# Kernel optimization log

Measured on AMD Instinct MI355X. Metric: run time of the kernel, lower is better.

The kernel has to match this reference:

```python
import jax, jax.numpy as jnp
import numpy as np

D_MODEL = 512; FPQ = 15; SEQ = 2048; BSZ = 2
D_STATE = 16; D_CONV = 4; HEADDIM = 64; NHEADS = 16
D_INNER = 1024; CONV_DIM = D_INNER + 2 * D_STATE
D_IN_PROJ = 2 * D_INNER + 2 * D_STATE + NHEADS  # 2096
D_FF = 2048  # mlp_ratio 4.0 * 512
EPS_GATE = 0.01


def _rmsnorm(x, w, eps):
    xf = x.astype(jnp.float32)
    v = jnp.mean(xf * xf, axis=-1, keepdims=True)
    return w * (xf * jax.lax.rsqrt(v + eps)).astype(x.dtype)


def _mamba2(x, inproj, convw, convb, dtbias, Alog, Dp, normw, outproj):
    b, l, _ = x.shape
    zxbcdt = x @ inproj.T                      # [b,l,2096]
    z = zxbcdt[..., :D_INNER]
    xBC = zxbcdt[..., D_INNER:D_INNER + CONV_DIM]
    dt = zxbcdt[..., D_INNER + CONV_DIM:]      # [b,l,h]
    # causal depthwise conv1d (kernel D_CONV) + SiLU
    xp = jnp.pad(xBC, ((0, 0), (D_CONV - 1, 0), (0, 0)))
    conv = convb + sum(xp[:, k:k + l, :] * convw[:, k] for k in range(D_CONV))
    xBC = jax.nn.silu(conv)
    xs = xBC[..., :D_INNER]
    Bm = xBC[..., D_INNER:D_INNER + D_STATE]   # [b,l,n]
    Cm = xBC[..., D_INNER + D_STATE:]          # [b,l,n]
    dt = jax.nn.softplus(dt + dtbias)          # [b,l,h]
    A = -jnp.exp(Alog)                         # [h]
    xh = xs.reshape(b, l, NHEADS, HEADDIM)     # [b,l,h,p]
    dA = jnp.exp(dt * A)                       # [b,l,h]

    def step(hst, inp):
        dA_t, dt_t, B_t, x_t, C_t = inp        # [b,h],[b,h],[b,n],[b,h,p],[b,n]
        hst = dA_t[:, :, None, None] * hst + jnp.einsum('bh,bn,bhp->bhpn', dt_t, B_t, x_t)
        return hst, jnp.einsum('bhpn,bn->bhp', hst, C_t)

    h0 = jnp.zeros((b, NHEADS, HEADDIM, D_STATE), x.dtype)
    _, ys = jax.lax.scan(step, h0, (dA.transpose(1, 0, 2), dt.transpose(1, 0, 2),
                                    Bm.transpose(1, 0, 2), xh.transpose(1, 0, 2, 3),
                                    Cm.transpose(1, 0, 2)))
    y = ys.transpose(1, 0, 2, 3) + Dp[None, None, :, None] * xh  # [b,l,h,p]
    y = y.reshape(b, l, D_INNER) * jax.nn.silu(z)                # gated
    y = _rmsnorm(y, normw, 1e-5)
    return y @ outproj.T


def _forward(hidden_states, norm1_w, wfc_w, wfc_b, gfc_w, gfc_b,
             f_inproj, f_convw, f_convb, f_dtbias, f_Alog, f_D, f_normw, f_outproj,
             b_inproj, b_convw, b_convb, b_dtbias, b_Alog, b_D, b_normw, b_outproj,
             norm2_w, fc1_w, fc1_b, fc2_w, fc2_b):
    residual = hidden_states
    h = _rmsnorm(hidden_states, norm1_w, 1e-6)
    bsz, seq_len, d = h.shape
    cq = FPQ + 1
    nck = seq_len // cq
    h4 = h.reshape(bsz, nck, cq, d)
    frames = h4[:, :, :FPQ, :]                       # [b,nc,FPQ,d]
    queries = h4[:, :, FPQ, :]                       # [b,nc,d]
    alpha = jax.nn.softmax(queries @ wfc_w.T + wfc_b, axis=-1)   # [b,nc,FPQ]
    agg = jnp.einsum('bcfd,bcf->bcd', frames, alpha)
    gate = jax.nn.sigmoid(queries @ gfc_w.T + gfc_b)             # [b,nc,1]
    gate = gate * (1 - 2 * EPS_GATE) + EPS_GATE
    qn = queries * (1 - gate) + agg * gate
    h4 = jnp.concatenate([frames, qn[:, :, None, :]], axis=2)
    h = h4.reshape(bsz, seq_len, d)
    out_fwd = _mamba2(h, f_inproj, f_convw, f_convb, f_dtbias, f_Alog, f_D, f_normw, f_outproj)
    out_bwd = jnp.flip(_mamba2(jnp.flip(h, 1), b_inproj, b_convw, b_convb, b_dtbias, b_Alog, b_D, b_normw, b_outproj), 1)
    h = out_fwd + out_bwd + residual
    rm = h
    h = _rmsnorm(h, norm2_w, 1e-6)
    h = jax.nn.silu(h @ fc1_w.T + fc1_b) @ fc2_w.T + fc2_b
    h = h + rm
    return h + residual


def setup_inputs() -> dict:
    key = jax.random.key(0)
    ks = jax.random.split(key, 16)

    def n(k, shape, s=0.02):
        return s * jax.random.normal(k, shape, jnp.float32)

    def mixer(kb):
        k = jax.random.split(kb, 6)
        dtv = jnp.exp(jax.random.uniform(k[3], (NHEADS,), minval=jnp.log(1e-3), maxval=jnp.log(0.1)))
        return dict(
            inproj=n(k[0], (D_IN_PROJ, D_MODEL)),
            convw=n(k[1], (CONV_DIM, D_CONV), 0.2),
            convb=jnp.zeros((CONV_DIM,), jnp.float32),
            dtbias=jnp.log(jnp.expm1(dtv)),
            Alog=jnp.log(jax.random.uniform(k[4], (NHEADS,), minval=1.0, maxval=16.0)),
            D=jnp.ones((NHEADS,), jnp.float32),
            normw=jnp.ones((D_INNER,), jnp.float32),
            outproj=n(k[2], (D_MODEL, D_INNER)),
        )

    mf = mixer(ks[1]); mb = mixer(ks[2])
    inp = {
        'hidden_states': jax.random.normal(ks[0], (BSZ, SEQ, D_MODEL), jnp.float32),
        'norm1_w': jnp.ones((D_MODEL,), jnp.float32),
        'wfc_w': n(ks[3], (FPQ, D_MODEL)) * 0.001,
        'wfc_b': jnp.zeros((FPQ,), jnp.float32),
        'gfc_w': n(ks[4], (1, D_MODEL)) * 0.001,
        'gfc_b': jnp.zeros((1,), jnp.float32),
        'norm2_w': jnp.ones((D_MODEL,), jnp.float32),
        'fc1_w': n(ks[5], (D_FF, D_MODEL)),
        'fc1_b': jnp.zeros((D_FF,), jnp.float32),
        'fc2_w': n(ks[6], (D_MODEL, D_FF)),
        'fc2_b': jnp.zeros((D_MODEL,), jnp.float32),
    }
    for pre, m in (('f_', mf), ('b_', mb)):
        for kname, v in m.items():
            inp[pre + kname] = v
    return inp


def reference(hidden_states, norm1_w, wfc_w, wfc_b, gfc_w, gfc_b,
              f_inproj, f_convw, f_convb, f_dtbias, f_Alog, f_D, f_normw, f_outproj,
              b_inproj, b_convw, b_convb, b_dtbias, b_Alog, b_D, b_normw, b_outproj,
              norm2_w, fc1_w, fc1_b, fc2_w, fc2_b):
    return _forward(hidden_states, norm1_w, wfc_w, wfc_b, gfc_w, gfc_b,
                    f_inproj, f_convw, f_convb, f_dtbias, f_Alog, f_D, f_normw, f_outproj,
                    b_inproj, b_convw, b_convb, b_dtbias, b_Alog, b_D, b_normw, b_outproj,
                    norm2_w, fc1_w, fc1_b, fc2_w, fc2_b)
```

## Files before the change

kernel.cpp:

```cpp
#include <hip/hip_runtime.h>
#include <math.h>

#define SEQ 2048
#define BSZ 2
#define DM 512
#define DIN 1024
#define DSTATE 16
#define NH 16
#define HD 64
#define CONVDIM 1056
#define DINPROJ 2096
#define DFF 2048
#define ROWS (BSZ*SEQ)
#define NCH 16
#define CT  (SEQ/NCH)
#define ZXBN 8388608ull
#define ZXTN 196608ull
#define XSN 4194304ull
#define BCN 65536ull
#define DTN 65536ull
#define YN  4194304ull
#define HSN 524288ull

typedef short bf16x8 __attribute__((ext_vector_type(8)));
typedef float f32x4  __attribute__((ext_vector_type(4)));

__device__ __forceinline__ float sigf(float x){ return 1.f/(1.f+expf(-x)); }

__device__ __forceinline__ unsigned short f2bf(float f){
  union { float f; unsigned u; } v; v.f = f;
  unsigned r = (v.u + 0x7FFFu + ((v.u >> 16) & 1u)) >> 16;
  return (unsigned short)r;
}
__device__ __forceinline__ float bf2f(unsigned short h){
  union { unsigned u; float f; } v; v.u = ((unsigned)h) << 16;
  return v.f;
}

template<int N> __device__ __forceinline__ void s_wait_vmcnt(){
  if constexpr (N == 0)      asm volatile("s_waitcnt vmcnt(0)" ::: "memory");
  else if constexpr (N == 1) asm volatile("s_waitcnt vmcnt(1)" ::: "memory");
  else if constexpr (N == 2) asm volatile("s_waitcnt vmcnt(2)" ::: "memory");
  else if constexpr (N == 3) asm volatile("s_waitcnt vmcnt(3)" ::: "memory");
  else if constexpr (N == 4) asm volatile("s_waitcnt vmcnt(4)" ::: "memory");
  else                       asm volatile("s_waitcnt vmcnt(8)" ::: "memory");
}

__device__ __forceinline__ float wave_reduce(float v){
#pragma unroll
  for (int o = 32; o > 0; o >>= 1) v += __shfl_down(v, o);
  return v;
}

__device__ __forceinline__ float block_reduce_256(float v, float* sbuf){
  v = wave_reduce(v);
  int lane = threadIdx.x & 63, wid = threadIdx.x >> 6;
  if (lane == 0) sbuf[wid] = v;
  __syncthreads();
  float s = sbuf[0] + sbuf[1] + sbuf[2] + sbuf[3];
  __syncthreads();
  return s;
}

struct Cast6 {
  const float* src[6];
  unsigned short* dst[6];
  int n[6];
};
__global__ __launch_bounds__(256)
void cast6_k(Cast6 cp){
  int seg = blockIdx.y;
  const float* src = cp.src[seg];
  unsigned short* dst = cp.dst[seg];
  int n4 = cp.n[seg] >> 2;
  int i = blockIdx.x*256 + threadIdx.x;
  if (i >= n4) return;
  float4 v = *(const float4*)&src[i*4];
  ushort4 o;
  o.x = f2bf(v.x); o.y = f2bf(v.y); o.z = f2bf(v.z); o.w = f2bf(v.w);
  *(ushort4*)&dst[i*4] = o;
}

__global__ __launch_bounds__(256)
void rmsnorm512_k(const float* __restrict__ x, const float* __restrict__ w,
                  float* __restrict__ y, unsigned short* __restrict__ yb, float eps){
  __shared__ float sbuf[4];
  int r = blockIdx.x;
  const float* xr = x + (size_t)r*DM;
  float v0 = xr[threadIdx.x];
  float v1 = xr[threadIdx.x + 256];
  float ss = block_reduce_256(v0*v0 + v1*v1, sbuf);
  float rs = rsqrtf(ss*(1.f/DM) + eps);
  float o0 = w[threadIdx.x]*v0*rs;
  float o1 = w[threadIdx.x+256]*v1*rs;
  y[(size_t)r*DM + threadIdx.x]       = o0;
  y[(size_t)r*DM + threadIdx.x + 256] = o1;
  yb[(size_t)r*DM + threadIdx.x]       = f2bf(o0);
  yb[(size_t)r*DM + threadIdx.x + 256] = f2bf(o1);
}

__global__ __launch_bounds__(256)
void gated_fusion_k(float* __restrict__ h, unsigned short* __restrict__ hb,
                    const float* __restrict__ wfc_w, const float* __restrict__ wfc_b,
                    const float* __restrict__ gfc_w, const float* __restrict__ gfc_b){
  int c = blockIdx.x;
  float* base = h + (size_t)c*16*DM;
  float* qrow = base + 15*DM;
  unsigned short* qrow_b = hb + (size_t)c*16*DM + 15*DM;
  __shared__ float q[DM];
  __shared__ float dots[16];
  for (int i = threadIdx.x; i < DM; i += 256) q[i] = qrow[i];
  __syncthreads();
  int wid = threadIdx.x >> 6, lane = threadIdx.x & 63;
  for (int f = wid; f < 16; f += 4){
    const float* wf = (f < 15) ? (wfc_w + (size_t)f*DM) : gfc_w;
    float s = 0.f;
    for (int i = lane; i < DM; i += 64) s += q[i]*wf[i];
    s = wave_reduce(s);
    if (lane == 0) dots[f] = s;
  }
  __syncthreads();
  if (threadIdx.x == 0){
    float mx = -1e30f;
    for (int f = 0; f < 15; f++){ dots[f] += wfc_b[f]; mx = fmaxf(mx, dots[f]); }
    float sum = 0.f;
    for (int f = 0; f < 15; f++){ float e = expf(dots[f]-mx); dots[f] = e; sum += e; }
    float inv = 1.f/sum;
    for (int f = 0; f < 15; f++) dots[f] *= inv;
    float g = sigf(dots[15] + gfc_b[0]);
    dots[15] = g*0.98f + 0.01f;
  }
  __syncthreads();
  float gate = dots[15];
  for (int d = threadIdx.x; d < DM; d += 256){
    float agg = 0.f;
#pragma unroll
    for (int f = 0; f < 15; f++) agg += base[(size_t)f*DM + d]*dots[f];
    float qn = q[d]*(1.f-gate) + agg*gate;
    qrow[d] = qn;
    qrow_b[d] = f2bf(qn);
  }
}

template<int NW, int WM, int WN, int FM, int FN, int DEPTH, int NBUF>
__global__ __launch_bounds__(NW*64)
void mgemm_k(const unsigned short* __restrict__ A, size_t Astride,
             const unsigned short* __restrict__ W0, const unsigned short* __restrict__ W1,
             const float* __restrict__ bias, const float* __restrict__ add1,
             const float* __restrict__ add2, float* __restrict__ Cf,
             unsigned short* __restrict__ Cb, size_t Cstride,
             int K, int Nreal, int flipArg, int act){
  constexpr int BM = WM*FM*16;
  constexpr int BN = WN*FN*16;
  constexpr int NG = (BM+BN)/16;
  constexpr int L  = NG/NW;
  static_assert(NG % NW == 0, "staging must be uniform per wave");
  constexpr int BUFS = (BM+BN)*32;
  __shared__ unsigned short S[NBUF*BUFS];
  int tid = threadIdx.x;
  int w = tid >> 6, lane = tid & 63;
  int gx = gridDim.x;
  int nwg = gx*gridDim.y;
  int bid = blockIdx.x + gx*blockIdx.y;
  int swz = (bid & 7)*(nwg >> 3) + (bid >> 3);
  int n0 = (swz % gx)*BN, m0 = (swz / gx)*BM;
  int dir = blockIdx.z;
  const unsigned short* Aa = A + (size_t)dir*Astride;
  const unsigned short* Wd = dir ? W1 : W0;
  int flip = (flipArg < 0) ? dir : flipArg;
  int wr = w / WN, wc = w % WN;

  f32x4 acc[FM][FN];
#pragma unroll
  for (int i = 0; i < FM; i++)
#pragma unroll
    for (int j = 0; j < FN; j++)
#pragma unroll
      for (int r = 0; r < 4; r++) acc[i][j][r] = 0.f;

  const unsigned short* gp[L];
  int gdst[L];
#pragma unroll
  for (int gi = 0; gi < L; gi++){
    int g = w + gi*NW;
    int r16 = lane >> 2, cch = lane & 3;
    int r = g*16 + r16;
    const unsigned short* src;
    if (r < BM){
      int gm = m0 + r;
      if (flip) gm = (gm & ~(SEQ-1)) | ((SEQ-1) - (gm & (SEQ-1)));
      src = Aa + (size_t)gm*K;
    } else {
      src = Wd + (size_t)(n0 + (r - BM))*K;
    }
    int c2 = (cch + ((r16 >> 1) & 3)) & 3;
    gp[gi] = src + c2*8;
    gdst[gi] = g*16*32;
  }
  int aoff[FM], boff[FN];
#pragma unroll
  for (int i = 0; i < FM; i++){
    int R = wr*FM*16 + i*16 + (lane & 15);
    int slot = ((lane >> 4) - ((R >> 1) & 3)) & 3;
    aoff[i] = R*32 + slot*8;
  }
#pragma unroll
  for (int j = 0; j < FN; j++){
    int R = BM + wc*FN*16 + j*16 + (lane & 15);
    int slot = ((lane >> 4) - ((R >> 1) & 3)) & 3;
    boff[j] = R*32 + slot*8;
  }

  int T = K >> 5;
#pragma unroll
  for (int jt = 0; jt < DEPTH; jt++){
#pragma unroll
    for (int gi = 0; gi < L; gi++)
      __builtin_amdgcn_global_load_lds(
        (const __attribute__((address_space(1))) void*)(gp[gi] + (jt << 5)),
        (__attribute__((address_space(3))) void*)&S[jt*BUFS + gdst[gi]], 16, 0, 0);
  }

  int cs = 0;
  for (int t = 0; t < T; t++){
    int rem = T - 1 - t;
    if (rem >= DEPTH-1)             s_wait_vmcnt<L*(DEPTH-1)>();
    else if constexpr (DEPTH >= 3){ if (rem == 1) s_wait_vmcnt<L>(); else s_wait_vmcnt<0>(); }
    else                            s_wait_vmcnt<0>();
    __builtin_amdgcn_s_barrier();
    __builtin_amdgcn_sched_barrier(0);
    const unsigned short* buf = &S[cs*BUFS];
    bf16x8 af[FM], bfr[FN];
#pragma unroll
    for (int i = 0; i < FM; i++) af[i] = *(const bf16x8*)&buf[aoff[i]];
#pragma unroll
    for (int j = 0; j < FN; j++) bfr[j] = *(const bf16x8*)&buf[boff[j]];
    if (t + DEPTH < T){
      int ss = cs + DEPTH; if (ss >= NBUF) ss -= NBUF;
#pragma unroll
      for (int gi = 0; gi < L; gi++)
        __builtin_amdgcn_global_load_lds(
          (const __attribute__((address_space(1))) void*)(gp[gi] + ((t + DEPTH) << 5)),
          (__attribute__((address_space(3))) void*)&S[ss*BUFS + gdst[gi]], 16, 0, 0);
    }
#pragma unroll
    for (int i = 0; i < FM; i++)
#pragma unroll
      for (int j = 0; j < FN; j++)
        acc[i][j] = __builtin_amdgcn_mfma_f32_16x16x32_bf16(af[i], bfr[j], acc[i][j], 0, 0, 0);
    cs = (cs + 1 == NBUF) ? 0 : cs + 1;
  }

  float* Cfd = Cf ? Cf + (size_t)dir*Cstride : nullptr;
  unsigned short* Cbd = Cb ? Cb + (size_t)dir*Cstride : nullptr;
  int mbase = m0 + wr*FM*16 + (lane >> 4)*4;
  int nbase = n0 + wc*FN*16 + (lane & 15);
#pragma unroll
  for (int i = 0; i < FM; i++){
#pragma unroll
    for (int j = 0; j < FN; j++){
      int col = nbase + j*16;
      if (col < Nreal){
        float bv = bias ? bias[col] : 0.f;
#pragma unroll
        for (int r = 0; r < 4; r++){
          size_t idx = (size_t)(mbase + i*16 + r)*Nreal + col;
          float x = acc[i][j][r] + bv;
          if (act) x = x*sigf(x);
          if (add1) x += add1[idx] + add2[idx];
          if (Cbd) Cbd[idx] = f2bf(x); else Cfd[idx] = x;
        }
      }
    }
  }
}

__global__ __launch_bounds__(512)
void skinny48_k(const float* __restrict__ hnorm,
                const float* __restrict__ W0, const float* __restrict__ W1,
                float* __restrict__ zxt){
  int dir = blockIdx.y;
  const float* W = dir ? W1 : W0;
  float* zt = zxt + (size_t)dir*ZXTN;
  int r0 = blockIdx.x*16;
  __shared__ float rows[16][DM];
#pragma unroll
  for (int rr = 0; rr < 16; rr++){
    int r = r0 + rr;
    int rf = dir ? ((r & ~(SEQ-1)) | ((SEQ-1) - (r & (SEQ-1)))) : r;
    rows[rr][threadIdx.x] = hnorm[(size_t)rf*DM + threadIdx.x];
  }
  __syncthreads();
  int wv = threadIdx.x >> 6, lane = threadIdx.x & 63;
  for (int c = wv; c < 48; c += 8){
    const float* wr = W + (size_t)(2048 + c)*DM;
    float wreg[8];
#pragma unroll
    for (int i = 0; i < 8; i++) wreg[i] = wr[lane + i*64];
    float part[16];
#pragma unroll
    for (int rr = 0; rr < 16; rr++){
      float s = 0.f;
#pragma unroll
      for (int i = 0; i < 8; i++) s = fmaf(rows[rr][lane + i*64], wreg[i], s);
      part[rr] = s;
    }
#pragma unroll
    for (int off = 32; off > 0; off >>= 1){
#pragma unroll
      for (int rr = 0; rr < 16; rr++) part[rr] += __shfl_down(part[rr], off);
    }
    if (lane == 0){
#pragma unroll
      for (int rr = 0; rr < 16; rr++) zt[(size_t)(r0+rr)*48 + c] = part[rr];
    }
  }
}

__global__ __launch_bounds__(256)
void conv_dt_k(const unsigned short* __restrict__ zxb, const float* __restrict__ zxt,
               const float* __restrict__ convw0, const float* __restrict__ convw1,
               const float* __restrict__ convb0, const float* __restrict__ convb1,
               const float* __restrict__ dtbias0, const float* __restrict__ dtbias1,
               const float* __restrict__ Alog0, const float* __restrict__ Alog1,
               unsigned short* __restrict__ xs, float* __restrict__ Bm, float* __restrict__ Cm,
               float* __restrict__ dtv, float* __restrict__ dAv){
  int dir = blockIdx.z;
  const unsigned short* zb = zxb + (size_t)dir*ZXBN;
  const float* zt = zxt + (size_t)dir*ZXTN;
  const float* convw = dir ? convw1 : convw0;
  const float* convb = dir ? convb1 : convb0;
  int r0 = blockIdx.y*4;
  int l0 = r0 & (SEQ-1);
  int rbase = r0 - l0;
  int c = blockIdx.x*256 + threadIdx.x;
  if (c < CONVDIM){
    float w0 = convw[c*4+0], w1 = convw[c*4+1], w2 = convw[c*4+2], w3 = convw[c*4+3];
    float bv = convb[c];
    float v[7];
#pragma unroll
    for (int i = 0; i < 7; i++){
      int ls = l0 - 3 + i;
      if (ls < 0) v[i] = 0.f;
      else if (c < DIN) v[i] = bf2f(zb[(size_t)(rbase+ls)*2048 + 1024 + c]);
      else v[i] = zt[(size_t)(rbase+ls)*48 + (c - DIN)];
    }
#pragma unroll
    for (int j = 0; j < 4; j++){
      float acc = bv + v[j]*w0 + v[j+1]*w1 + v[j+2]*w2 + v[j+3]*w3;
      float val = acc*sigf(acc);
      int r = r0 + j;
      if (c < DIN) xs[(size_t)dir*XSN + (size_t)r*DIN + c] = f2bf(val);
      else if (c < DIN + DSTATE) Bm[(size_t)dir*BCN + (size_t)r*DSTATE + (c - DIN)] = val;
      else Cm[(size_t)dir*BCN + (size_t)r*DSTATE + (c - DIN - DSTATE)] = val;
    }
  } else if (blockIdx.x == 4 && threadIdx.x >= 64 && threadIdx.x < 128){
    const float* dtbias = dir ? dtbias1 : dtbias0;
    const float* Alog   = dir ? Alog1 : Alog0;
    int i = threadIdx.x - 64;
    int j = i >> 4, hh = i & 15;
    int r = r0 + j;
    float x = zt[(size_t)r*48 + 32 + hh] + dtbias[hh];
    float sp = (x > 20.f) ? x : log1pf(expf(x));
    dtv[(size_t)dir*DTN + (size_t)r*NH + hh] = sp;
    dAv[(size_t)dir*DTN + (size_t)r*NH + hh] = expf(-expf(Alog[hh])*sp);
  }
}

__global__ __launch_bounds__(64)
void scanA_k(const unsigned short* __restrict__ xs, const float* __restrict__ Bm,
             const float* __restrict__ Cm, const float* __restrict__ dtv,
             const float* __restrict__ dAv, float* __restrict__ y,
             float* __restrict__ Hs, float* __restrict__ Ps){
  int gb = blockIdx.x;
  int dir = gb >> 9;
  int idx = gb & 511;
  int c = idx & (NCH-1);
  int h = (idx >> 4) & 15;
  int b = idx >> 8;
  int p = threadIdx.x;
  int t0 = c*CT;
  __shared__ __align__(16) float sB[CT][16];
  __shared__ __align__(16) float sC[CT][16];
  __shared__ float sdt[CT];
  __shared__ float sdA[CT];
  const unsigned short* xb = xs + (size_t)dir*XSN + ((size_t)b*SEQ + t0)*DIN + h*HD;
  float*       yb  = y  + (size_t)dir*YN  + ((size_t)b*SEQ + t0)*DIN + h*HD;
  const float* Bb  = Bm + (size_t)dir*BCN + ((size_t)b*SEQ + t0)*DSTATE;
  const float* Cb  = Cm + (size_t)dir*BCN + ((size_t)b*SEQ + t0)*DSTATE;
  const float* dtb = dtv + (size_t)dir*DTN + ((size_t)b*SEQ + t0)*NH + h;
  const float* dAb = dAv + (size_t)dir*DTN + ((size_t)b*SEQ + t0)*NH + h;
#pragma unroll
  for (int k = 0; k < (CT*16)/64; k++){
    int i = p + k*64;
    ((float*)sB)[i] = Bb[i];
    ((float*)sC)[i] = Cb[i];
  }
#pragma unroll
  for (int k = 0; k < CT/64; k++){
    int i = p + k*64;
    sdt[i] = dtb[(size_t)i*NH];
    sdA[i] = dAb[(size_t)i*NH];
  }
  __syncthreads();

  float hst[16];
#pragma unroll
  for (int n = 0; n < 16; n++) hst[n] = 0.f;
  float P = 1.f;
  float xcur[16], xnxt[16];
#pragma unroll
  for (int j = 0; j < 16; j++) xcur[j] = bf2f(xb[(size_t)j*DIN + p]);

  for (int tt = 0; tt < CT; tt += 16){
    bool pf = (tt + 16 < CT);
    if (pf){
#pragma unroll
      for (int j = 0; j < 16; j++) xnxt[j] = bf2f(xb[(size_t)(tt+16+j)*DIN + p]);
    }
#pragma unroll
    for (int j = 0; j < 16; j++){
      int t = tt + j;
      float xv = xcur[j]*sdt[t];
      float dA = sdA[t];
      P *= dA;
      float4 b0 = *(const float4*)&sB[t][0];
      float4 b1 = *(const float4*)&sB[t][4];
      float4 b2 = *(const float4*)&sB[t][8];
      float4 b3 = *(const float4*)&sB[t][12];
      hst[0]  = fmaf(dA, hst[0],  b0.x*xv);
      hst[1]  = fmaf(dA, hst[1],  b0.y*xv);
      hst[2]  = fmaf(dA, hst[2],  b0.z*xv);
      hst[3]  = fmaf(dA, hst[3],  b0.w*xv);
      hst[4]  = fmaf(dA, hst[4],  b1.x*xv);
      hst[5]  = fmaf(dA, hst[5],  b1.y*xv);
      hst[6]  = fmaf(dA, hst[6],  b1.z*xv);
      hst[7]  = fmaf(dA, hst[7],  b1.w*xv);
      hst[8]  = fmaf(dA, hst[8],  b2.x*xv);
      hst[9]  = fmaf(dA, hst[9],  b2.y*xv);
      hst[10] = fmaf(dA, hst[10], b2.z*xv);
      hst[11] = fmaf(dA, hst[11], b2.w*xv);
      hst[12] = fmaf(dA, hst[12], b3.x*xv);
      hst[13] = fmaf(dA, hst[13], b3.y*xv);
      hst[14] = fmaf(dA, hst[14], b3.z*xv);
      hst[15] = fmaf(dA, hst[15], b3.w*xv);
      float4 c0 = *(const float4*)&sC[t][0];
      float4 c1 = *(const float4*)&sC[t][4];
      float4 c2 = *(const float4*)&sC[t][8];
      float4 c3 = *(const float4*)&sC[t][12];
      float a0 = hst[0]*c0.x;  a0 = fmaf(hst[1],  c0.y, a0);
      a0 = fmaf(hst[2],  c0.z, a0); a0 = fmaf(hst[3],  c0.w, a0);
      float a1 = hst[4]*c1.x;  a1 = fmaf(hst[5],  c1.y, a1);
      a1 = fmaf(hst[6],  c1.z, a1); a1 = fmaf(hst[7],  c1.w, a1);
      float a2 = hst[8]*c2.x;  a2 = fmaf(hst[9],  c2.y, a2);
      a2 = fmaf(hst[10], c2.z, a2); a2 = fmaf(hst[11], c2.w, a2);
      float a3 = hst[12]*c3.x; a3 = fmaf(hst[13], c3.y, a3);
      a3 = fmaf(hst[14], c3.z, a3); a3 = fmaf(hst[15], c3.w, a3);
      yb[(size_t)t*DIN + p] = (a0+a1)+(a2+a3);
    }
    if (pf){
#pragma unroll
      for (int j = 0; j < 16; j++) xcur[j] = xnxt[j];
    }
  }
  size_t base = (size_t)dir*HSN + ((size_t)((b*NH + h)*NCH + c))*1024;
#pragma unroll
  for (int n = 0; n < 16; n++) Hs[base + n*64 + p] = hst[n];
  if (p == 0) Ps[dir*512 + (b*NH + h)*NCH + c] = P;
}

__global__ __launch_bounds__(64)
void scanC_k(const float* __restrict__ Cm, const float* __restrict__ dAv,
             const float* __restrict__ Hs, const float* __restrict__ Ps,
             float* __restrict__ y){
  int gb = blockIdx.x;
  int dir = gb >> 9;
  int idx = gb & 511;
  int c = idx & (NCH-1);
  if (c == 0) return;
  int h = (idx >> 4) & 15;
  int b = idx >> 8;
  int p = threadIdx.x;
  int t0 = c*CT;
  int bh = b*NH + h;
  float hstart[16];
#pragma unroll
  for (int n = 0; n < 16; n++) hstart[n] = 0.f;
  for (int j = 0; j < c; j++){
    float Pj = Ps[dir*512 + bh*NCH + j];
    const float* Hj = Hs + (size_t)dir*HSN + ((size_t)(bh*NCH + j))*1024;
#pragma unroll
    for (int n = 0; n < 16; n++) hstart[n] = fmaf(Pj, hstart[n], Hj[n*64 + p]);
  }
  __shared__ __align__(16) float sC[CT][16];
  __shared__ float sdA[CT];
  const float* Cb  = Cm + (size_t)dir*BCN + ((size_t)b*SEQ + t0)*DSTATE;
  const float* dAb = dAv + (size_t)dir*DTN + ((size_t)b*SEQ + t0)*NH + h;
  float*       yb  = y  + (size_t)dir*YN  + ((size_t)b*SEQ + t0)*DIN + h*HD;
#pragma unroll
  for (int k = 0; k < (CT*16)/64; k++){
    int i = p + k*64;
    ((float*)sC)[i] = Cb[i];
  }
#pragma unroll
  for (int k = 0; k < CT/64; k++){
    int i = p + k*64;
    sdA[i] = dAb[(size_t)i*NH];
  }
  __syncthreads();

  float cp = 1.f;
  float ycur[16], ynxt[16];
#pragma unroll
  for (int j = 0; j < 16; j++) ycur[j] = yb[(size_t)j*DIN + p];
  for (int tt = 0; tt < CT; tt += 16){
    bool pf = (tt + 16 < CT);
    if (pf){
#pragma unroll
      for (int j = 0; j < 16; j++) ynxt[j] = yb[(size_t)(tt+16+j)*DIN + p];
    }
#pragma unroll
    for (int j = 0; j < 16; j++){
      int t = tt + j;
      cp *= sdA[t];
      float4 c0 = *(const float4*)&sC[t][0];
      float4 c1 = *(const float4*)&sC[t][4];
      float4 c2 = *(const float4*)&sC[t][8];
      float4 c3 = *(const float4*)&sC[t][12];
      float a0 = hstart[0]*c0.x;  a0 = fmaf(hstart[1],  c0.y, a0);
      a0 = fmaf(hstart[2],  c0.z, a0); a0 = fmaf(hstart[3],  c0.w, a0);
      float a1 = hstart[4]*c1.x;  a1 = fmaf(hstart[5],  c1.y, a1);
      a1 = fmaf(hstart[6],  c1.z, a1); a1 = fmaf(hstart[7],  c1.w, a1);
      float a2 = hstart[8]*c2.x;  a2 = fmaf(hstart[9],  c2.y, a2);
      a2 = fmaf(hstart[10], c2.z, a2); a2 = fmaf(hstart[11], c2.w, a2);
      float a3 = hstart[12]*c3.x; a3 = fmaf(hstart[13], c3.y, a3);
      a3 = fmaf(hstart[14], c3.z, a3); a3 = fmaf(hstart[15], c3.w, a3);
      float dot = (a0+a1)+(a2+a3);
      yb[(size_t)t*DIN + p] = ycur[j] + cp*dot;
    }
    if (pf){
#pragma unroll
      for (int j = 0; j < 16; j++) ycur[j] = ynxt[j];
    }
  }
}

__global__ __launch_bounds__(256)
void gated_rms_k(const float* __restrict__ y, const unsigned short* __restrict__ xs,
                 const unsigned short* __restrict__ zxb,
                 const float* __restrict__ Dp0, const float* __restrict__ Dp1,
                 const float* __restrict__ nw0, const float* __restrict__ nw1,
                 unsigned short* __restrict__ out){
  __shared__ float sbuf[4];
  int r = blockIdx.x;
  int dir = blockIdx.y;
  const float* Dp = dir ? Dp1 : Dp0;
  const float* normw = dir ? nw1 : nw0;
  const float* yr = y + (size_t)dir*YN + (size_t)r*DIN;
  const unsigned short* xr = xs + (size_t)dir*XSN + (size_t)r*DIN;
  const unsigned short* zr = zxb + (size_t)dir*ZXBN + (size_t)r*2048;
  unsigned short* outr = out + (size_t)dir*((size_t)ROWS*DIN) + (size_t)r*DIN;
  int d0 = threadIdx.x*4;
  float4 yv4 = *(const float4*)&yr[d0];
  ushort4 xu4 = *(const ushort4*)&xr[d0];
  ushort4 zu4 = *(const ushort4*)&zr[d0];
  float Dv = Dp[d0 >> 6];
  float vals[4]; float ss = 0.f;
  float yv[4] = {yv4.x, yv4.y, yv4.z, yv4.w};
  float xv[4] = {bf2f(xu4.x), bf2f(xu4.y), bf2f(xu4.z), bf2f(xu4.w)};
  float zv[4] = {bf2f(zu4.x), bf2f(zu4.y), bf2f(zu4.z), bf2f(zu4.w)};
#pragma unroll
  for (int i = 0; i < 4; i++){
    float g = (yv[i] + Dv*xv[i]) * (zv[i]*sigf(zv[i]));
    vals[i] = g; ss += g*g;
  }
  ss = block_reduce_256(ss, sbuf);
  float rs = rsqrtf(ss*(1.f/DIN) + 1e-5f);
  ushort4 o;
  o.x = f2bf(normw[d0+0]*vals[0]*rs);
  o.y = f2bf(normw[d0+1]*vals[1]*rs);
  o.z = f2bf(normw[d0+2]*vals[2]*rs);
  o.w = f2bf(normw[d0+3]*vals[3]*rs);
  *(ushort4*)&outr[d0] = o;
}

__global__ __launch_bounds__(256)
void addres_rms_k(const float* __restrict__ outf, const float* __restrict__ outb,
                  const float* __restrict__ hid, const float* __restrict__ w,
                  float* __restrict__ hsum, unsigned short* __restrict__ h2b){
  __shared__ float sbuf[4];
  int r = blockIdx.x;
  int l = r & (SEQ-1);
  int rb = (r - l) + ((SEQ-1) - l);
  float vals[2]; float ss = 0.f;
#pragma unroll
  for (int i = 0; i < 2; i++){
    int d = threadIdx.x + i*256;
    float v = outf[(size_t)r*DM + d] + outb[(size_t)rb*DM + d] + hid[(size_t)r*DM + d];
    hsum[(size_t)r*DM + d] = v;
    vals[i] = v; ss += v*v;
  }
  ss = block_reduce_256(ss, sbuf);
  float rs = rsqrtf(ss*(1.f/DM) + 1e-6f);
#pragma unroll
  for (int i = 0; i < 2; i++){
    int d = threadIdx.x + i*256;
    h2b[(size_t)r*DM + d] = f2bf(w[d]*vals[i]*rs);
  }
}

extern "C" void kernel_launch(void* const* d_in, const int* in_sizes, int n_in,
                              void* d_out, int out_size, void* d_ws, size_t ws_size,
                              hipStream_t stream){
  const float* hid     = (const float*)d_in[0];
  const float* norm1_w = (const float*)d_in[1];
  const float* wfc_w   = (const float*)d_in[2];
  const float* wfc_b   = (const float*)d_in[3];
  const float* gfc_w   = (const float*)d_in[4];
  const float* gfc_b   = (const float*)d_in[5];
  const float* norm2_w = (const float*)d_in[6];
  const float* fc1_w   = (const float*)d_in[7];
  const float* fc1_b   = (const float*)d_in[8];
  const float* fc2_w   = (const float*)d_in[9];
  const float* fc2_b   = (const float*)d_in[10];
  const float* inproj[2]  = {(const float*)d_in[11], (const float*)d_in[19]};
  const float* convw[2]   = {(const float*)d_in[12], (const float*)d_in[20]};
  const float* convb[2]   = {(const float*)d_in[13], (const float*)d_in[21]};
  const float* dtbias[2]  = {(const float*)d_in[14], (const float*)d_in[22]};
  const float* Alog[2]    = {(const float*)d_in[15], (const float*)d_in[23]};
  const float* Dp[2]      = {(const float*)d_in[16], (const float*)d_in[24]};
  const float* normw[2]   = {(const float*)d_in[17], (const float*)d_in[25]};
  const float* outproj[2] = {(const float*)d_in[18], (const float*)d_in[26]};

  float* ws = (float*)d_ws;
  unsigned short* zxb = (unsigned short*)ws;
  float* zxt   = ws + 8388608;
  float* xsf   = zxt + 2*ZXTN;
  unsigned short* xsb = (unsigned short*)xsf;
  float* Bmb   = xsf + 2*XSN;
  float* Cmb   = Bmb + 2*BCN;
  float* dtv   = Cmb + 2*BCN;
  float* dAv   = dtv + 2*DTN;
  float* ysc   = dAv + 2*DTN;
  float* outd  = ysc + 2*YN;
  float* hsum  = outd + 4194304;
  float* hnorm = hsum + 2097152;
  unsigned short* hnorm_bf = (unsigned short*)(hnorm + 2097152);
  unsigned short* ysc_bf   = (unsigned short*)(hnorm + 2097152 + 1048576);
  unsigned short* wbf      = (unsigned short*)(hnorm + 2097152 + 1048576 + 4194304);
  float* Hs = hsum;
  float* Ps = hsum + 2*HSN;
  unsigned short* a1_bf = (unsigned short*)zxb;
  unsigned short* h2_bf = xsb;
  unsigned short* wi0 = wbf,            * wi1 = wbf + 1048576;
  unsigned short* wo0 = wbf + 2097152,  * wo1 = wbf + 2621440;
  unsigned short* wf1 = wbf + 3145728;
  unsigned short* wf2 = wbf + 4194304;
  size_t need_bytes = (size_t)44957696*4;
  if (ws_size < need_bytes) return;

  Cast6 cp;
  cp.src[0] = inproj[0]; cp.dst[0] = wi0; cp.n[0] = 2048*512;
  cp.src[1] = inproj[1]; cp.dst[1] = wi1; cp.n[1] = 2048*512;
  cp.src[2] = outproj[0]; cp.dst[2] = wo0; cp.n[2] = 512*1024;
  cp.src[3] = outproj[1]; cp.dst[3] = wo1; cp.n[3] = 512*1024;
  cp.src[4] = fc1_w; cp.dst[4] = wf1; cp.n[4] = 2048*512;
  cp.src[5] = fc2_w; cp.dst[5] = wf2; cp.n[5] = 512*2048;
  cast6_k<<<dim3((2048*512/4)/256, 6), 256, 0, stream>>>(cp);

  rmsnorm512_k<<<ROWS, 256, 0, stream>>>(hid, norm1_w, hnorm, hnorm_bf, 1e-6f);
  gated_fusion_k<<<BSZ*(SEQ/16), 256, 0, stream>>>(hnorm, hnorm_bf, wfc_w, wfc_b, gfc_w, gfc_b);

  mgemm_k<8,2,4,4,2,2,3><<<dim3(2048/128, 4096/128, 2), 512, 0, stream>>>(
      hnorm_bf, 0, wi0, wi1, nullptr, nullptr, nullptr, nullptr, zxb, ZXBN,
      512, 2048, -1, 0);
  skinny48_k<<<dim3(ROWS/16, 2), 512, 0, stream>>>(hnorm, inproj[0], inproj[1], zxt);
  conv_dt_k<<<dim3(5, ROWS/4, 2), 256, 0, stream>>>(
      zxb, zxt, convw[0], convw[1], convb[0], convb[1], dtbias[0], dtbias[1],
      Alog[0], Alog[1], xsb, Bmb, Cmb, dtv, dAv);
  scanA_k<<<2*BSZ*NH*NCH, 64, 0, stream>>>(xsb, Bmb, Cmb, dtv, dAv, ysc, Hs, Ps);
  scanC_k<<<2*BSZ*NH*NCH, 64, 0, stream>>>(Cmb, dAv, Hs, Ps, ysc);
  gated_rms_k<<<dim3(ROWS, 2), 256, 0, stream>>>(
      ysc, xsb, zxb, Dp[0], Dp[1], normw[0], normw[1], ysc_bf);
  mgemm_k<8,2,4,2,1,3,4><<<dim3(512/64, 4096/64, 2), 512, 0, stream>>>(
      ysc_bf, (size_t)ROWS*DIN, wo0, wo1, nullptr, nullptr, nullptr,
      outd, nullptr, 2097152, 1024, DM, 0, 0);

  addres_rms_k<<<ROWS, 256, 0, stream>>>(outd, outd + 2097152, hid, norm2_w, hsum, h2_bf);
  mgemm_k<8,2,4,4,2,2,3><<<dim3(2048/128, 4096/128, 1), 512, 0, stream>>>(
      h2_bf, 0, wf1, wf1, fc1_b, nullptr, nullptr, nullptr, a1_bf, 0,
      512, DFF, 0, 1);
  mgemm_k<8,2,4,2,1,3,4><<<dim3(512/64, 4096/64, 1), 512, 0, stream>>>(
      a1_bf, 0, wf2, wf2, fc2_b, hsum, hid, (float*)d_out, nullptr, 0,
      2048, DM, 0, 0);
}
```

Measured before the change: 237.7 us.

## Store scan outputs in bf16 and retune GEMM pipeline depth/buffers

```diff
diff --git a/kernel.cpp b/kernel.cpp
--- a/kernel.cpp
+++ b/kernel.cpp
@@ -235,6 +235,11 @@
     for (int i = 0; i < FM; i++) af[i] = *(const bf16x8*)&buf[aoff[i]];
 #pragma unroll
     for (int j = 0; j < FN; j++) bfr[j] = *(const bf16x8*)&buf[boff[j]];
+    if constexpr (NBUF == DEPTH){
+      asm volatile("s_waitcnt lgkmcnt(0)" ::: "memory");
+      __builtin_amdgcn_sched_barrier(0);
+      __builtin_amdgcn_s_barrier();
+    }
     if (t + DEPTH < T){
       int ss = cs + DEPTH; if (ss >= NBUF) ss -= NBUF;
 #pragma unroll
@@ -370,7 +375,7 @@
 __global__ __launch_bounds__(64)
 void scanA_k(const unsigned short* __restrict__ xs, const float* __restrict__ Bm,
              const float* __restrict__ Cm, const float* __restrict__ dtv,
-             const float* __restrict__ dAv, float* __restrict__ y,
+             const float* __restrict__ dAv, unsigned short* __restrict__ y,
              float* __restrict__ Hs, float* __restrict__ Ps){
   int gb = blockIdx.x;
   int dir = gb >> 9;
@@ -385,7 +390,7 @@
   __shared__ float sdt[CT];
   __shared__ float sdA[CT];
   const unsigned short* xb = xs + (size_t)dir*XSN + ((size_t)b*SEQ + t0)*DIN + h*HD;
-  float*       yb  = y  + (size_t)dir*YN  + ((size_t)b*SEQ + t0)*DIN + h*HD;
+  unsigned short* yb = y + (size_t)dir*YN + ((size_t)b*SEQ + t0)*DIN + h*HD;
   const float* Bb  = Bm + (size_t)dir*BCN + ((size_t)b*SEQ + t0)*DSTATE;
   const float* Cb  = Cm + (size_t)dir*BCN + ((size_t)b*SEQ + t0)*DSTATE;
   const float* dtb = dtv + (size_t)dir*DTN + ((size_t)b*SEQ + t0)*NH + h;
@@ -456,7 +461,7 @@
       a2 = fmaf(hst[10], c2.z, a2); a2 = fmaf(hst[11], c2.w, a2);
       float a3 = hst[12]*c3.x; a3 = fmaf(hst[13], c3.y, a3);
       a3 = fmaf(hst[14], c3.z, a3); a3 = fmaf(hst[15], c3.w, a3);
-      yb[(size_t)t*DIN + p] = (a0+a1)+(a2+a3);
+      yb[(size_t)t*DIN + p] = f2bf((a0+a1)+(a2+a3));
     }
     if (pf){
 #pragma unroll
@@ -472,7 +477,7 @@
 __global__ __launch_bounds__(64)
 void scanC_k(const float* __restrict__ Cm, const float* __restrict__ dAv,
              const float* __restrict__ Hs, const float* __restrict__ Ps,
-             float* __restrict__ y){
+             unsigned short* __restrict__ y){
   int gb = blockIdx.x;
   int dir = gb >> 9;
   int idx = gb & 511;
@@ -496,7 +501,7 @@
   __shared__ float sdA[CT];
   const float* Cb  = Cm + (size_t)dir*BCN + ((size_t)b*SEQ + t0)*DSTATE;
   const float* dAb = dAv + (size_t)dir*DTN + ((size_t)b*SEQ + t0)*NH + h;
-  float*       yb  = y  + (size_t)dir*YN  + ((size_t)b*SEQ + t0)*DIN + h*HD;
+  unsigned short* yb = y + (size_t)dir*YN + ((size_t)b*SEQ + t0)*DIN + h*HD;
 #pragma unroll
   for (int k = 0; k < (CT*16)/64; k++){
     int i = p + k*64;
@@ -512,12 +517,12 @@
   float cp = 1.f;
   float ycur[16], ynxt[16];
 #pragma unroll
-  for (int j = 0; j < 16; j++) ycur[j] = yb[(size_t)j*DIN + p];
+  for (int j = 0; j < 16; j++) ycur[j] = bf2f(yb[(size_t)j*DIN + p]);
   for (int tt = 0; tt < CT; tt += 16){
     bool pf = (tt + 16 < CT);
     if (pf){
 #pragma unroll
-      for (int j = 0; j < 16; j++) ynxt[j] = yb[(size_t)(tt+16+j)*DIN + p];
+      for (int j = 0; j < 16; j++) ynxt[j] = bf2f(yb[(size_t)(tt+16+j)*DIN + p]);
     }
 #pragma unroll
     for (int j = 0; j < 16; j++){
@@ -536,7 +541,7 @@
       float a3 = hstart[12]*c3.x; a3 = fmaf(hstart[13], c3.y, a3);
       a3 = fmaf(hstart[14], c3.z, a3); a3 = fmaf(hstart[15], c3.w, a3);
       float dot = (a0+a1)+(a2+a3);
-      yb[(size_t)t*DIN + p] = ycur[j] + cp*dot;
+      yb[(size_t)t*DIN + p] = f2bf(ycur[j] + cp*dot);
     }
     if (pf){
 #pragma unroll
@@ -546,7 +551,7 @@
 }
 
 __global__ __launch_bounds__(256)
-void gated_rms_k(const float* __restrict__ y, const unsigned short* __restrict__ xs,
+void gated_rms_k(const unsigned short* __restrict__ y, const unsigned short* __restrict__ xs,
                  const unsigned short* __restrict__ zxb,
                  const float* __restrict__ Dp0, const float* __restrict__ Dp1,
                  const float* __restrict__ nw0, const float* __restrict__ nw1,
@@ -556,17 +561,17 @@
   int dir = blockIdx.y;
   const float* Dp = dir ? Dp1 : Dp0;
   const float* normw = dir ? nw1 : nw0;
-  const float* yr = y + (size_t)dir*YN + (size_t)r*DIN;
+  const unsigned short* yr = y + (size_t)dir*YN + (size_t)r*DIN;
   const unsigned short* xr = xs + (size_t)dir*XSN + (size_t)r*DIN;
   const unsigned short* zr = zxb + (size_t)dir*ZXBN + (size_t)r*2048;
   unsigned short* outr = out + (size_t)dir*((size_t)ROWS*DIN) + (size_t)r*DIN;
   int d0 = threadIdx.x*4;
-  float4 yv4 = *(const float4*)&yr[d0];
+  ushort4 yu4 = *(const ushort4*)&yr[d0];
   ushort4 xu4 = *(const ushort4*)&xr[d0];
   ushort4 zu4 = *(const ushort4*)&zr[d0];
   float Dv = Dp[d0 >> 6];
   float vals[4]; float ss = 0.f;
-  float yv[4] = {yv4.x, yv4.y, yv4.z, yv4.w};
+  float yv[4] = {bf2f(yu4.x), bf2f(yu4.y), bf2f(yu4.z), bf2f(yu4.w)};
   float xv[4] = {bf2f(xu4.x), bf2f(xu4.y), bf2f(xu4.z), bf2f(xu4.w)};
   float zv[4] = {bf2f(zu4.x), bf2f(zu4.y), bf2f(zu4.z), bf2f(zu4.w)};
 #pragma unroll
@@ -642,6 +647,7 @@
   float* dtv   = Cmb + 2*BCN;
   float* dAv   = dtv + 2*DTN;
   float* ysc   = dAv + 2*DTN;
+  unsigned short* ysc_b = (unsigned short*)ysc;
   float* outd  = ysc + 2*YN;
   float* hsum  = outd + 4194304;
   float* hnorm = hsum + 2097152;
@@ -671,23 +677,23 @@
   rmsnorm512_k<<<ROWS, 256, 0, stream>>>(hid, norm1_w, hnorm, hnorm_bf, 1e-6f);
   gated_fusion_k<<<BSZ*(SEQ/16), 256, 0, stream>>>(hnorm, hnorm_bf, wfc_w, wfc_b, gfc_w, gfc_b);
 
-  mgemm_k<8,2,4,4,2,2,3><<<dim3(2048/128, 4096/128, 2), 512, 0, stream>>>(
+  mgemm_k<8,2,4,4,2,2,2><<<dim3(2048/128, 4096/128, 2), 512, 0, stream>>>(
       hnorm_bf, 0, wi0, wi1, nullptr, nullptr, nullptr, nullptr, zxb, ZXBN,
       512, 2048, -1, 0);
   skinny48_k<<<dim3(ROWS/16, 2), 512, 0, stream>>>(hnorm, inproj[0], inproj[1], zxt);
   conv_dt_k<<<dim3(5, ROWS/4, 2), 256, 0, stream>>>(
       zxb, zxt, convw[0], convw[1], convb[0], convb[1], dtbias[0], dtbias[1],
       Alog[0], Alog[1], xsb, Bmb, Cmb, dtv, dAv);
-  scanA_k<<<2*BSZ*NH*NCH, 64, 0, stream>>>(xsb, Bmb, Cmb, dtv, dAv, ysc, Hs, Ps);
-  scanC_k<<<2*BSZ*NH*NCH, 64, 0, stream>>>(Cmb, dAv, Hs, Ps, ysc);
+  scanA_k<<<2*BSZ*NH*NCH, 64, 0, stream>>>(xsb, Bmb, Cmb, dtv, dAv, ysc_b, Hs, Ps);
+  scanC_k<<<2*BSZ*NH*NCH, 64, 0, stream>>>(Cmb, dAv, Hs, Ps, ysc_b);
   gated_rms_k<<<dim3(ROWS, 2), 256, 0, stream>>>(
-      ysc, xsb, zxb, Dp[0], Dp[1], normw[0], normw[1], ysc_bf);
+      ysc_b, xsb, zxb, Dp[0], Dp[1], normw[0], normw[1], ysc_bf);
   mgemm_k<8,2,4,2,1,3,4><<<dim3(512/64, 4096/64, 2), 512, 0, stream>>>(
       ysc_bf, (size_t)ROWS*DIN, wo0, wo1, nullptr, nullptr, nullptr,
       outd, nullptr, 2097152, 1024, DM, 0, 0);
 
   addres_rms_k<<<ROWS, 256, 0, stream>>>(outd, outd + 2097152, hid, norm2_w, hsum, h2_bf);
-  mgemm_k<8,2,4,4,2,2,3><<<dim3(2048/128, 4096/128, 1), 512, 0, stream>>>(
+  mgemm_k<8,2,4,4,2,3,3><<<dim3(2048/128, 4096/128, 1), 512, 0, stream>>>(
       h2_bf, 0, wf1, wf1, fc1_b, nullptr, nullptr, nullptr, a1_bf, 0,
       512, DFF, 0, 1);
   mgemm_k<8,2,4,2,1,3,4><<<dim3(512/64, 4096/64, 1), 512, 0, stream>>>(
```

Result: no change. 239.0 us (+0.5%).
